# Kernel optimization log

Hardware: AMD Instinct MI355X
Metric: run time of the kernel (lower is better)

The kernel has to match this reference:

```python
import jax, jax.numpy as jnp
import numpy as np

D_MODEL = 1024
NUM_HEADS = 16
D_K = D_MODEL // NUM_HEADS
D_FF = 4096
EPS = 1e-5


def setup_inputs() -> dict:
    key = jax.random.key(0)
    ks = jax.random.split(key, 10)
    B, S = 4, 2048
    s = 1.0 / np.sqrt(D_MODEL)
    inp = {
        'x': jax.random.normal(ks[0], (B, S, D_MODEL), dtype=jnp.float32),
        'mask': jnp.ones((B, 1, 1, S), dtype=jnp.int32),
        'W_q': jax.random.normal(ks[1], (D_MODEL, D_MODEL), jnp.float32) * s,
        'W_k': jax.random.normal(ks[2], (D_MODEL, D_MODEL), jnp.float32) * s,
        'W_v': jax.random.normal(ks[3], (D_MODEL, D_MODEL), jnp.float32) * s,
        'W_o': jax.random.normal(ks[4], (D_MODEL, D_MODEL), jnp.float32) * s,
        'W1': jax.random.normal(ks[5], (D_MODEL, D_FF), jnp.float32) * s,
        'b1': jnp.zeros((D_FF,), jnp.float32),
        'W2': jax.random.normal(ks[6], (D_FF, D_MODEL), jnp.float32) * (1.0 / np.sqrt(D_FF)),
        'b2': jnp.zeros((D_MODEL,), jnp.float32),
        'g1': jnp.ones((D_MODEL,), jnp.float32),
        'be1': jnp.zeros((D_MODEL,), jnp.float32),
        'g2': jnp.ones((D_MODEL,), jnp.float32),
        'be2': jnp.zeros((D_MODEL,), jnp.float32),
    }
    return inp


def _layernorm(x, g, b):
    mu = jnp.mean(x, axis=-1, keepdims=True)
    var = jnp.mean(jnp.square(x - mu), axis=-1, keepdims=True)
    return (x - mu) * jax.lax.rsqrt(var + EPS) * g + b


def reference(x, mask, W_q, W_k, W_v, W_o, W1, b1, W2, b2, g1, be1, g2, be2):
    B, S, _ = x.shape
    def split(h):  # [B,S,D] -> [B,H,S,dk]
        return h.reshape(B, S, NUM_HEADS, D_K).transpose(0, 2, 1, 3)
    q = split(x @ W_q)
    k = split(x @ W_k)
    v = split(x @ W_v)
    scores = jnp.einsum('bhqd,bhkd->bhqk', q, k) / np.sqrt(D_K)
    scores = jnp.where(mask == 0, jnp.float32(-1e9), scores)
    attn = jax.nn.softmax(scores, axis=-1)
    ctx = jnp.einsum('bhqk,bhkd->bhqd', attn, v)
    ctx = ctx.transpose(0, 2, 1, 3).reshape(B, S, D_MODEL)
    z = ctx @ W_o
    # dropout in eval mode = identity
    z1 = _layernorm(z + x, g1, be1)
    ffn = jax.nn.relu(z1 @ W1 + b1) @ W2 + b2
    z2 = _layernorm(ffn + z1, g2, be2)
    return z2
```

## Files before the change

kernel.cpp:

```cpp
#include <hip/hip_runtime.h>

typedef __attribute__((ext_vector_type(4))) float f32x4;
typedef __bf16 bf16x8 __attribute__((ext_vector_type(8)));
typedef __bf16 bf16x4 __attribute__((ext_vector_type(4)));
typedef __attribute__((ext_vector_type(8))) unsigned short us8;
typedef __attribute__((ext_vector_type(4))) unsigned short us4;

#define DEV __device__ __forceinline__

DEV unsigned short f2bf(float f) {
    unsigned int u = __builtin_bit_cast(unsigned int, f);
    u += 0x7fffu + ((u >> 16) & 1u);
    return (unsigned short)(u >> 16);
}

DEV float ex2(float x) { return __builtin_amdgcn_exp2f(x); }

#define GLOAD16(gp, lp) __builtin_amdgcn_global_load_lds( \
    (const __attribute__((address_space(1))) void*)(gp),  \
    (__attribute__((address_space(3))) void*)(lp), 16, 0, 0)

template<int EPI>
__global__ __launch_bounds__(256) void gemm_bt(
    const unsigned short* __restrict__ A,
    const unsigned short* __restrict__ Bt,
    float* __restrict__ Cf,
    unsigned short* __restrict__ Cb,
    const float* __restrict__ res,
    const float* __restrict__ bias,
    int M, int N, int K)
{
    __shared__ unsigned short As[128 * 64];
    __shared__ unsigned short Bs[128 * 64];
    const int tid  = threadIdx.x;
    const int wave = tid >> 6;
    const int lane = tid & 63;
    const int bm = blockIdx.x * 128;
    const int bn = blockIdx.y * 128;
    const int wm = (wave >> 1) * 64;
    const int wn = (wave & 1) * 64;

    f32x4 acc[4][4];
#pragma unroll
    for (int i = 0; i < 4; ++i)
#pragma unroll
        for (int j = 0; j < 4; ++j) acc[i][j] = (f32x4){0.f, 0.f, 0.f, 0.f};

    const int srow = wave * 32 + (lane >> 3);
    const int scol = (lane & 7) * 8;
    const unsigned short* Ag = A + (size_t)(bm + srow) * K + scol;
    const unsigned short* Bg = Bt + (size_t)(bn + srow) * K + scol;
    unsigned short* AsBase = &As[(wave * 32) * 64];
    unsigned short* BsBase = &Bs[(wave * 32) * 64];

    const int nkt = K >> 6;
    for (int kt = 0; kt < nkt; ++kt) {
        if (kt) __syncthreads();
        const unsigned short* a0 = Ag + kt * 64;
        const unsigned short* b0 = Bg + kt * 64;
#pragma unroll
        for (int j = 0; j < 4; ++j) {
            GLOAD16(a0 + (size_t)j * 8 * K, AsBase + j * 8 * 64);
            GLOAD16(b0 + (size_t)j * 8 * K, BsBase + j * 8 * 64);
        }
        __syncthreads();
#pragma unroll
        for (int kk = 0; kk < 2; ++kk) {
            const int ko = kk * 32 + (lane >> 4) * 8;
            bf16x8 af[4], bf[4];
#pragma unroll
            for (int i = 0; i < 4; ++i)
                af[i] = *(const bf16x8*)&As[(wm + i * 16 + (lane & 15)) * 64 + ko];
#pragma unroll
            for (int j = 0; j < 4; ++j)
                bf[j] = *(const bf16x8*)&Bs[(wn + j * 16 + (lane & 15)) * 64 + ko];
#pragma unroll
            for (int i = 0; i < 4; ++i)
#pragma unroll
                for (int j = 0; j < 4; ++j)
                    acc[i][j] = __builtin_amdgcn_mfma_f32_16x16x32_bf16(af[i], bf[j], acc[i][j], 0, 0, 0);
        }
    }

    const int r0 = (lane >> 4) * 4;
    const int cn = lane & 15;
#pragma unroll
    for (int i = 0; i < 4; ++i) {
#pragma unroll
        for (int j = 0; j < 4; ++j) {
            const int gcol = bn + wn + j * 16 + cn;
#pragma unroll
            for (int r = 0; r < 4; ++r) {
                const int grow = bm + wm + i * 16 + r0 + r;
                const size_t off = (size_t)grow * N + gcol;
                float v = acc[i][j][r];
                if (EPI == 0) {
                    if (gcol < 1024) v *= 0.18033688f;
                    Cb[off] = f2bf(v);
                } else if (EPI == 1) {
                    Cf[off] = v + res[off];
                } else if (EPI == 2) {
                    v += bias[gcol];
                    Cb[off] = f2bf(fmaxf(v, 0.f));
                } else {
                    Cf[off] = v + bias[gcol] + res[off];
                }
            }
        }
    }
}

__global__ __launch_bounds__(256) void attn_fwd(
    const unsigned short* __restrict__ qkv,
    const unsigned short* __restrict__ vT,
    unsigned short* __restrict__ ctx)
{
    const int S = 2048, LD = 3072;
    const int tid = threadIdx.x, wave = tid >> 6, lane = tid & 63;
    const int swz = (blockIdx.x & 7) * 128 + (blockIdx.x >> 3);
    const int qb = swz & 15, bh = swz >> 4;
    const int b = bh >> 4, h = bh & 15;
    const int g = lane >> 4;
    const int qi = lane & 15;
    __shared__ unsigned short Pls[128 * 72];
    const int q0 = qb * 128 + wave * 32;

    bf16x8 qf[2][2];
#pragma unroll
    for (int mt = 0; mt < 2; ++mt)
#pragma unroll
        for (int kk = 0; kk < 2; ++kk)
            qf[mt][kk] = *(const bf16x8*)(qkv +
                (size_t)(b * S + q0 + mt * 16 + qi) * LD + h * 64 + kk * 32 + g * 8);

    f32x4 o[2][4];
#pragma unroll
    for (int mt = 0; mt < 2; ++mt)
#pragma unroll
        for (int dt = 0; dt < 4; ++dt) o[mt][dt] = (f32x4){0.f, 0.f, 0.f, 0.f};
    float mr[2] = {-3.0e38f, -3.0e38f};
    float lr[2] = {0.f, 0.f};

    const unsigned short* Kb0 = qkv + (size_t)(b * S) * LD + 1024 + h * 64;
    const unsigned short* Vb0 = vT + (size_t)(bh * 64) * S;
    unsigned short* Pw = &Pls[(wave * 32 + qi) * 72];

    for (int t = 0; t < 32; ++t) {
        f32x4 s[2][4];
#pragma unroll
        for (int mt = 0; mt < 2; ++mt)
#pragma unroll
            for (int nt = 0; nt < 4; ++nt) s[mt][nt] = (f32x4){0.f, 0.f, 0.f, 0.f};
#pragma unroll
        for (int kk = 0; kk < 2; ++kk) {
            bf16x8 kf[4];
#pragma unroll
            for (int nt = 0; nt < 4; ++nt)
                kf[nt] = *(const bf16x8*)(Kb0 +
                    (size_t)(t * 64 + nt * 16 + qi) * LD + kk * 32 + g * 8);
#pragma unroll
            for (int mt = 0; mt < 2; ++mt)
#pragma unroll
                for (int nt = 0; nt < 4; ++nt)
                    s[mt][nt] = __builtin_amdgcn_mfma_f32_16x16x32_bf16(kf[nt], qf[mt][kk], s[mt][nt], 0, 0, 0);
        }

        float mx[2];
#pragma unroll
        for (int mt = 0; mt < 2; ++mt) {
            float m0 = fmaxf(fmaxf(s[mt][0][0], s[mt][0][1]), fmaxf(s[mt][0][2], s[mt][0][3]));
#pragma unroll
            for (int nt = 1; nt < 4; ++nt) {
                m0 = fmaxf(m0, fmaxf(fmaxf(s[mt][nt][0], s[mt][nt][1]),
                                     fmaxf(s[mt][nt][2], s[mt][nt][3])));
            }
            m0 = fmaxf(m0, __shfl_xor(m0, 16));
            m0 = fmaxf(m0, __shfl_xor(m0, 32));
            mx[mt] = m0;
        }
        const int need = __any((mx[0] > mr[0] + 8.f) || (mx[1] > mr[1] + 8.f));
        if (need) {
#pragma unroll
            for (int mt = 0; mt < 2; ++mt) {
                const float mn = fmaxf(mr[mt], mx[mt]);
                const float al = ex2(mr[mt] - mn);
                mr[mt] = mn;
                lr[mt] *= al;
#pragma unroll
                for (int i = 0; i < 4; ++i) {
                    const float ar = __shfl(al, (lane & 48) + g * 4 + i);
#pragma unroll
                    for (int dt = 0; dt < 4; ++dt) o[mt][dt][i] *= ar;
                }
            }
        }
#pragma unroll
        for (int mt = 0; mt < 2; ++mt) {
            float sum = 0.f;
#pragma unroll
            for (int nt = 0; nt < 4; ++nt) {
                float p0 = ex2(s[mt][nt][0] - mr[mt]);
                float p1 = ex2(s[mt][nt][1] - mr[mt]);
                float p2 = ex2(s[mt][nt][2] - mr[mt]);
                float p3 = ex2(s[mt][nt][3] - mr[mt]);
                sum += (p0 + p1) + (p2 + p3);
                bf16x4 pb = {(__bf16)p0, (__bf16)p1, (__bf16)p2, (__bf16)p3};
                *(bf16x4*)&Pw[mt * 16 * 72 + nt * 16 + g * 4] = pb;
            }
            sum += __shfl_xor(sum, 16);
            sum += __shfl_xor(sum, 32);
            lr[mt] += sum;
        }

#pragma unroll
        for (int kk = 0; kk < 2; ++kk) {
            bf16x8 pa[2], vb[4];
#pragma unroll
            for (int mt = 0; mt < 2; ++mt)
                pa[mt] = *(const bf16x8*)&Pw[mt * 16 * 72 + kk * 32 + g * 8];
#pragma unroll
            for (int dt = 0; dt < 4; ++dt)
                vb[dt] = *(const bf16x8*)(Vb0 +
                    (size_t)(dt * 16 + qi) * S + t * 64 + kk * 32 + g * 8);
#pragma unroll
            for (int mt = 0; mt < 2; ++mt)
#pragma unroll
                for (int dt = 0; dt < 4; ++dt)
                    o[mt][dt] = __builtin_amdgcn_mfma_f32_16x16x32_bf16(pa[mt], vb[dt], o[mt][dt], 0, 0, 0);
        }
    }

#pragma unroll
    for (int mt = 0; mt < 2; ++mt) {
#pragma unroll
        for (int i = 0; i < 4; ++i) {
            const float linv = 1.f / __shfl(lr[mt], (lane & 48) + g * 4 + i);
            const int q = q0 + mt * 16 + g * 4 + i;
#pragma unroll
            for (int dt = 0; dt < 4; ++dt)
                ctx[(size_t)(b * S + q) * 1024 + h * 64 + dt * 16 + qi] =
                    f2bf(o[mt][dt][i] * linv);
        }
    }
}

template<int DUAL>
__global__ __launch_bounds__(256) void ln_k(
    const float* __restrict__ in, const float* __restrict__ g,
    const float* __restrict__ be, float* __restrict__ of,
    unsigned short* __restrict__ ob)
{
    const int row = blockIdx.x;
    const int tid = threadIdx.x;
    const int lane = tid & 63, wave = tid >> 6;
    const float4 v = ((const float4*)(in + (size_t)row * 1024))[tid];
    float s  = v.x + v.y + v.z + v.w;
    float s2 = v.x * v.x + v.y * v.y + v.z * v.z + v.w * v.w;
#pragma unroll
    for (int m = 1; m <= 32; m <<= 1) { s += __shfl_xor(s, m); s2 += __shfl_xor(s2, m); }
    __shared__ float red[8];
    if (lane == 0) { red[wave] = s; red[wave + 4] = s2; }
    __syncthreads();
    const float mu  = (red[0] + red[1] + red[2] + red[3]) * (1.f / 1024.f);
    const float e2  = (red[4] + red[5] + red[6] + red[7]) * (1.f / 1024.f);
    const float rstd = rsqrtf(e2 - mu * mu + 1e-5f);
    const float4 gv = ((const float4*)g)[tid];
    const float4 bv = ((const float4*)be)[tid];
    float4 r;
    r.x = (v.x - mu) * rstd * gv.x + bv.x;
    r.y = (v.y - mu) * rstd * gv.y + bv.y;
    r.z = (v.z - mu) * rstd * gv.z + bv.z;
    r.w = (v.w - mu) * rstd * gv.w + bv.w;
    ((float4*)(of + (size_t)row * 1024))[tid] = r;
    if (DUAL) {
        us4 ub = {f2bf(r.x), f2bf(r.y), f2bf(r.z), f2bf(r.w)};
        ((us4*)(ob + (size_t)row * 1024))[tid] = ub;
    }
}

__global__ __launch_bounds__(256) void wtrans(
    const float* __restrict__ W, unsigned short* __restrict__ Wt, int K, int N)
{
    __shared__ float t[32][33];
    const int n0 = blockIdx.x * 32, k0 = blockIdx.y * 32;
    const int c = threadIdx.x & 31, rr = threadIdx.x >> 5;
#pragma unroll
    for (int p = 0; p < 4; ++p)
        t[rr + p * 8][c] = W[(size_t)(k0 + rr + p * 8) * N + n0 + c];
    __syncthreads();
#pragma unroll
    for (int p = 0; p < 4; ++p)
        Wt[(size_t)(n0 + rr + p * 8) * K + k0 + c] = f2bf(t[c][rr + p * 8]);
}

__global__ __launch_bounds__(256) void vtrans(
    const unsigned short* __restrict__ qkv, unsigned short* __restrict__ vT)
{
    __shared__ unsigned short t[32][33];
    const int s0 = blockIdx.x * 32;
    const int d0 = blockIdx.y * 32;
    const int bh = blockIdx.z, b = bh >> 4, h = bh & 15;
    const int c = threadIdx.x & 31, rr = threadIdx.x >> 5;
#pragma unroll
    for (int p = 0; p < 4; ++p)
        t[rr + p * 8][c] = qkv[(size_t)(b * 2048 + s0 + rr + p * 8) * 3072 + 2048 + h * 64 + d0 + c];
    __syncthreads();
#pragma unroll
    for (int p = 0; p < 4; ++p)
        vT[(size_t)(bh * 64 + d0 + rr + p * 8) * 2048 + s0 + c] = t[c][rr + p * 8];
}

__global__ __launch_bounds__(256) void cvt_x(
    const float* __restrict__ x, unsigned short* __restrict__ xb)
{
    const int i = blockIdx.x * 256 + threadIdx.x;
    const float4 v = ((const float4*)x)[i];
    us4 ub = {f2bf(v.x), f2bf(v.y), f2bf(v.z), f2bf(v.w)};
    ((us4*)xb)[i] = ub;
}

extern "C" void kernel_launch(void* const* d_in, const int* in_sizes, int n_in,
                              void* d_out, int out_size, void* d_ws, size_t ws_size,
                              hipStream_t stream)
{
    const float* x   = (const float*)d_in[0];
    const float* Wq  = (const float*)d_in[2];
    const float* Wk  = (const float*)d_in[3];
    const float* Wv  = (const float*)d_in[4];
    const float* Wo  = (const float*)d_in[5];
    const float* W1  = (const float*)d_in[6];
    const float* b1  = (const float*)d_in[7];
    const float* W2  = (const float*)d_in[8];
    const float* b2  = (const float*)d_in[9];
    const float* g1  = (const float*)d_in[10];
    const float* be1 = (const float*)d_in[11];
    const float* g2  = (const float*)d_in[12];
    const float* be2 = (const float*)d_in[13];
    float* out = (float*)d_out;

    char* ws = (char*)d_ws;
    size_t off = 0;
    auto alloc = [&](size_t bytes) {
        char* p = ws + off;
        off += (bytes + 255) & ~(size_t)255;
        return p;
    };
    unsigned short* xb    = (unsigned short*)alloc(8192ull * 1024 * 2);
    unsigned short* Wqkvt = (unsigned short*)alloc(3072ull * 1024 * 2);
    unsigned short* Wot   = (unsigned short*)alloc(1024ull * 1024 * 2);
    unsigned short* W1t   = (unsigned short*)alloc(4096ull * 1024 * 2);
    unsigned short* W2t   = (unsigned short*)alloc(1024ull * 4096 * 2);
    unsigned short* qkv   = (unsigned short*)alloc(8192ull * 3072 * 2);
    unsigned short* vT    = (unsigned short*)alloc(64ull * 64 * 2048 * 2);
    unsigned short* ctx   = (unsigned short*)alloc(8192ull * 1024 * 2);
    float* z1 = (float*)alloc(8192ull * 1024 * 4);
    unsigned short* h1 = (unsigned short*)alloc(8192ull * 4096 * 2);
    float* zres = (float*)qkv;
    unsigned short* z1b = xb;
    float* ffn = (float*)vT;

    cvt_x<<<8192, 256, 0, stream>>>(x, xb);
    wtrans<<<dim3(32, 32), 256, 0, stream>>>(Wq, Wqkvt, 1024, 1024);
    wtrans<<<dim3(32, 32), 256, 0, stream>>>(Wk, Wqkvt + 1024 * 1024, 1024, 1024);
    wtrans<<<dim3(32, 32), 256, 0, stream>>>(Wv, Wqkvt + 2048 * 1024, 1024, 1024);
    wtrans<<<dim3(32, 32), 256, 0, stream>>>(Wo, Wot, 1024, 1024);
    wtrans<<<dim3(128, 32), 256, 0, stream>>>(W1, W1t, 1024, 4096);
    wtrans<<<dim3(32, 128), 256, 0, stream>>>(W2, W2t, 4096, 1024);

    gemm_bt<0><<<dim3(64, 24), 256, 0, stream>>>(xb, Wqkvt, nullptr, qkv,
                                                 nullptr, nullptr, 8192, 3072, 1024);
    vtrans<<<dim3(64, 2, 64), 256, 0, stream>>>(qkv, vT);
    attn_fwd<<<1024, 256, 0, stream>>>(qkv, vT, ctx);
    gemm_bt<1><<<dim3(64, 8), 256, 0, stream>>>(ctx, Wot, zres, nullptr,
                                                x, nullptr, 8192, 1024, 1024);
    ln_k<1><<<8192, 256, 0, stream>>>(zres, g1, be1, z1, z1b);
    gemm_bt<2><<<dim3(64, 32), 256, 0, stream>>>(z1b, W1t, nullptr, h1,
                                                 nullptr, b1, 8192, 4096, 1024);
    gemm_bt<3><<<dim3(64, 8), 256, 0, stream>>>(h1, W2t, ffn, nullptr,
                                                z1, b2, 8192, 1024, 4096);
    ln_k<0><<<8192, 256, 0, stream>>>(ffn, g2, be2, out, nullptr);
}
```

Before: 710.8 us.

## Stage K and V tiles through double-buffered LDS in attention kernel

The attention kernel used to have each wave read K and V fragments straight from global memory, so all four waves re-fetched the same tiles. Each 64-row K/V tile is now loaded once per block into LDS with async global_load_lds into an XOR-swizzled layout. The next tile is prefetched into the second buffer while the current one is consumed. This cuts redundant global and L2 traffic and hides load latency, at the cost of a block-wide barrier per iteration and more LDS, which may lower occupancy.

Result: faster. 602.4 us (-15.2%).

```diff
diff --git a/kernel.cpp b/kernel.cpp
--- a/kernel.cpp
+++ b/kernel.cpp
@@ -122,6 +122,8 @@
     const int b = bh >> 4, h = bh & 15;
     const int g = lane >> 4;
     const int qi = lane & 15;
+    __shared__ unsigned short Kls[2][64 * 64];
+    __shared__ unsigned short Vls[2][64 * 64];
     __shared__ unsigned short Pls[128 * 72];
     const int q0 = qb * 128 + wave * 32;
 
@@ -145,7 +147,29 @@
     const unsigned short* Vb0 = vT + (size_t)(bh * 64) * S;
     unsigned short* Pw = &Pls[(wave * 32 + qi) * 72];
 
+    const int srow0 = wave * 16;
+    const int srw = lane >> 3;
+    const int sck = lane & 7;
+    auto STAGE = [&](int tt, int bb) {
+#pragma unroll
+        for (int j = 0; j < 2; ++j) {
+            const int r = srow0 + j * 8 + srw;
+            const int cg = (sck ^ (r & 7)) * 8;
+            GLOAD16(Kb0 + (size_t)(tt * 64 + r) * LD + cg,
+                    &Kls[bb][(srow0 + j * 8) * 64]);
+            GLOAD16(Vb0 + (size_t)r * S + tt * 64 + cg,
+                    &Vls[bb][(srow0 + j * 8) * 64]);
+        }
+    };
+
+    STAGE(0, 0);
+    __syncthreads();
+
     for (int t = 0; t < 32; ++t) {
+        const int cur = t & 1;
+        if (t < 31) STAGE(t + 1, cur ^ 1);
+
+        const int xr = (qi & 7);
         f32x4 s[2][4];
 #pragma unroll
         for (int mt = 0; mt < 2; ++mt)
@@ -153,11 +177,11 @@
             for (int nt = 0; nt < 4; ++nt) s[mt][nt] = (f32x4){0.f, 0.f, 0.f, 0.f};
 #pragma unroll
         for (int kk = 0; kk < 2; ++kk) {
+            const int ck = ((kk * 4 + g) ^ xr) * 8;
             bf16x8 kf[4];
 #pragma unroll
             for (int nt = 0; nt < 4; ++nt)
-                kf[nt] = *(const bf16x8*)(Kb0 +
-                    (size_t)(t * 64 + nt * 16 + qi) * LD + kk * 32 + g * 8);
+                kf[nt] = *(const bf16x8*)&Kls[cur][(nt * 16 + qi) * 64 + ck];
 #pragma unroll
             for (int mt = 0; mt < 2; ++mt)
 #pragma unroll
@@ -214,20 +238,22 @@
 
 #pragma unroll
         for (int kk = 0; kk < 2; ++kk) {
+            const int ck = ((kk * 4 + g) ^ xr) * 8;
             bf16x8 pa[2], vb[4];
 #pragma unroll
             for (int mt = 0; mt < 2; ++mt)
                 pa[mt] = *(const bf16x8*)&Pw[mt * 16 * 72 + kk * 32 + g * 8];
 #pragma unroll
             for (int dt = 0; dt < 4; ++dt)
-                vb[dt] = *(const bf16x8*)(Vb0 +
-                    (size_t)(dt * 16 + qi) * S + t * 64 + kk * 32 + g * 8);
+                vb[dt] = *(const bf16x8*)&Vls[cur][(dt * 16 + qi) * 64 + ck];
 #pragma unroll
             for (int mt = 0; mt < 2; ++mt)
 #pragma unroll
                 for (int dt = 0; dt < 4; ++dt)
                     o[mt][dt] = __builtin_amdgcn_mfma_f32_16x16x32_bf16(pa[mt], vb[dt], o[mt][dt], 0, 0, 0);
         }
+
+        __syncthreads();
     }
 
 #pragma unroll
```
